# Performance work log

Hardware: AMD Instinct MI355X
Metric: run time of the kernel (lower is better)

Reference implementation:

```python
import jax, jax.numpy as jnp
import numpy as np

FACTOR = 0.1   # init_kwargs factor
EPS = 1e-7
B, C, H, W = 256, 3, 224, 224


def setup_inputs() -> dict:
    key = jax.random.key(0)
    k1, k2, k3 = jax.random.split(key, 3)
    x = jax.random.normal(k1, (B, C, H, W), dtype=jnp.float32)
    shift_fy = jax.random.uniform(k2, (B,), dtype=jnp.float32)  # maps to torch.rand(1)
    shift_fx = jax.random.uniform(k3, (B,), dtype=jnp.float32)
    return {"x": x, "shift_fy": shift_fy, "shift_fx": shift_fx}


def _shift_axis(img, shift, axis, size):
    # Equivalent to torch in-place slice copy + zero-fill:
    #   shift>0: img[..., :size-shift] = img[..., shift:]; img[..., size-shift:] = 0
    #   shift<0: img[..., -shift:]   = img[..., :shift];  img[..., :-shift]   = 0
    # == roll by -shift, then zero positions j where j+shift is out of [0, size)
    idx = jnp.arange(size)
    rolled = jnp.roll(img, -shift, axis=axis)
    mask = (idx + shift >= 0) & (idx + shift < size)
    shp = [1, 1, 1]
    shp[axis] = size
    return rolled * mask.reshape(shp).astype(img.dtype)


def _per_image(img, fy, fx):
    # img: [C, H, W]
    h, w = img.shape[1], img.shape[2]
    # int(shift_factor * size) truncates toward zero -> jnp.trunc
    sy = jnp.trunc((fy * 2.0 - 1.0) * FACTOR * h).astype(jnp.int32)
    sx = jnp.trunc((fx * 2.0 - 1.0) * FACTOR * w).astype(jnp.int32)
    img = _shift_axis(img, sy, 1, h)
    img = _shift_axis(img, sx, 2, w)
    # standardize with unbiased std (torch.std default, ddof=1)
    n = img.size
    mean = jnp.mean(img)
    var = jnp.sum(jnp.square(img - mean)) / (n - 1)
    img = (img - mean) / (jnp.sqrt(var) + EPS)
    # min-max normalize
    mn = jnp.min(img)
    mx = jnp.max(img)
    return (img - mn) / (mx - mn)


def reference(x, shift_fy, shift_fx):
    # fully vectorized over the batch (original uses a Python per-image loop)
    return jax.vmap(_per_image)(x, shift_fy, shift_fx)
```

## Files before the change

### kernel.cpp

```cpp
#include <hip/hip_runtime.h>
#include <math.h>


constexpr int kC = 3, kH = 224, kW = 224;
constexpr int kCHW  = kC * kH * kW;
constexpr int kROWS = kC * kH;
constexpr int kQPR  = kW / 4;
constexpr int TB    = 1024;
constexpr int WVB   = TB / 64;
constexpr int RPW   = kROWS / WVB;

typedef float f32x4 __attribute__((ext_vector_type(4)));

template <int NB>
__device__ __forceinline__ void p1_batch(const float* __restrict__ xb,
                                         int t0, int wv, int i0,
                                         const float* cm, int rlo, int rhi,
                                         float& vmin, float& vmax)
{
    f32x4 v[NB];
    #pragma unroll
    for (int u = 0; u < NB; ++u) {
        const int rr = wv + (t0 + u) * WVB;
        v[u] = *(const f32x4*)(xb + rr * kW + i0);
    }
    #pragma unroll
    for (int u = 0; u < NB; ++u) {
        const int rr = wv + (t0 + u) * WVB;
        const int j  = rr % kH;
        const float srm = (j >= rlo && j < rhi) ? 1.0f : 0.0f;
        #pragma unroll
        for (int k = 0; k < 4; ++k) {
            const float val = v[u][k] * cm[k] * srm;
            vmin = fminf(vmin, val);
            vmax = fmaxf(vmax, val);
        }
    }
}

template <int NB, int R>
__device__ __forceinline__ void p2_batch(const float* __restrict__ xb,
                                         float* __restrict__ ob,
                                         int t0, int wv, int i0, int qa, int qb,
                                         const float* cm, int sy,
                                         float inv, float zoff)
{
    f32x4 av[NB], bv[NB];
    #pragma unroll
    for (int u = 0; u < NB; ++u) {
        const int rr = wv + (t0 + u) * WVB;
        const int j  = rr % kH;
        const int jj = j + sy;
        const int jc = ((unsigned)jj < (unsigned)kH) ? jj : j;
        const float* __restrict__ src = xb + (rr - j + jc) * kW;
        av[u] = *(const f32x4*)(src + qa);
        bv[u] = *(const f32x4*)(src + qb);
    }
    #pragma unroll
    for (int u = 0; u < NB; ++u) {
        const int rr = wv + (t0 + u) * WVB;
        const int j  = rr % kH;
        const int jj = j + sy;
        const float scale = ((unsigned)jj < (unsigned)kH) ? inv : 0.0f;
        f32x4 o;
        #pragma unroll
        for (int k = 0; k < 4; ++k) {
            const float sel = (k + R < 4) ? av[u][k + R] : bv[u][k + R - 4];
            o[k] = fmaf(sel * cm[k], scale, zoff);
        }
        *(f32x4*)(ob + rr * kW + i0) = o;
    }
}

template <int R>
__device__ __forceinline__ void phase2(const float* __restrict__ xb,
                                       float* __restrict__ ob,
                                       int sy, int sx, float inv, float zoff,
                                       int wv, int lane)
{
    if (lane >= kQPR) return;
    const int i0   = lane * 4;
    const int base = i0 + sx - R;
    int qa = base;     qa = qa < 0 ? 0 : qa; qa = qa > kW - 4 ? kW - 4 : qa;
    int qb = base + 4; qb = qb < 0 ? 0 : qb; qb = qb > kW - 4 ? kW - 4 : qb;

    float cm[4];
    #pragma unroll
    for (int k = 0; k < 4; ++k)
        cm[k] = ((unsigned)(i0 + k + sx) < (unsigned)kW) ? 1.0f : 0.0f;

    for (int t0 = 0; t0 < RPW - 2; t0 += 4)
        p2_batch<4, R>(xb, ob, t0, wv, i0, qa, qb, cm, sy, inv, zoff);
    p2_batch<2, R>(xb, ob, RPW - 2, wv, i0, qa, qb, cm, sy, inv, zoff);
}

__global__ __launch_bounds__(TB) void shift_norm(
    const float* __restrict__ x, const float* __restrict__ sfy,
    const float* __restrict__ sfx, float* __restrict__ out)
{
    const int img = blockIdx.x;
    const float* __restrict__ xb = x + (size_t)img * kCHW;
    float* __restrict__ ob = out + (size_t)img * kCHW;

    float ty = sfy[img] * 2.0f - 1.0f; ty *= 0.1f; ty *= (float)kH;
    const int sy = (int)truncf(ty);
    float tx = sfx[img] * 2.0f - 1.0f; tx *= 0.1f; tx *= (float)kW;
    const int sx = (int)truncf(tx);

    const int rlo = sy > 0 ? sy : 0;
    const int rhi = kH + (sy < 0 ? sy : 0);
    const int clo = sx > 0 ? sx : 0;
    const int chi = kW + (sx < 0 ? sx : 0);

    const int tid  = threadIdx.x;
    const int lane = tid & 63;
    const int wv   = __builtin_amdgcn_readfirstlane(tid >> 6);

    const bool hasfill = (sy != 0) | (sx != 0);
    float vmin = hasfill ? 0.0f : INFINITY;
    float vmax = hasfill ? 0.0f : -INFINITY;

    if (lane < kQPR) {
        const int i0 = lane * 4;
        float cm[4];
        #pragma unroll
        for (int k = 0; k < 4; ++k)
            cm[k] = ((i0 + k) >= clo && (i0 + k) < chi) ? 1.0f : 0.0f;

        for (int t0 = 0; t0 < RPW - 2; t0 += 8)
            p1_batch<8>(xb, t0, wv, i0, cm, rlo, rhi, vmin, vmax);
        p1_batch<2>(xb, RPW - 2, wv, i0, cm, rlo, rhi, vmin, vmax);
    }

    #pragma unroll
    for (int off = 32; off > 0; off >>= 1) {
        vmin = fminf(vmin, __shfl_down(vmin, off));
        vmax = fmaxf(vmax, __shfl_down(vmax, off));
    }
    __shared__ float smin[WVB], smax[WVB];
    __shared__ float s_mn, s_inv;
    if (lane == 0) { smin[tid >> 6] = vmin; smax[tid >> 6] = vmax; }
    __syncthreads();
    if (tid == 0) {
        float mn = smin[0], mx = smax[0];
        #pragma unroll
        for (int w = 1; w < WVB; ++w) {
            mn = fminf(mn, smin[w]);
            mx = fmaxf(mx, smax[w]);
        }
        s_mn  = mn;
        s_inv = 1.0f / (mx - mn);
    }
    __syncthreads();
    const float mn   = s_mn;
    const float inv  = s_inv;
    const float zoff = (0.0f - mn) * inv;

    switch (sx & 3) {
        case 0: phase2<0>(xb, ob, sy, sx, inv, zoff, wv, lane); break;
        case 1: phase2<1>(xb, ob, sy, sx, inv, zoff, wv, lane); break;
        case 2: phase2<2>(xb, ob, sy, sx, inv, zoff, wv, lane); break;
        default: phase2<3>(xb, ob, sy, sx, inv, zoff, wv, lane); break;
    }
}

extern "C" void kernel_launch(void* const* d_in, const int* in_sizes, int n_in,
                              void* d_out, int out_size, void* d_ws, size_t ws_size,
                              hipStream_t stream) {
    const float* x  = (const float*)d_in[0];
    const float* fy = (const float*)d_in[1];
    const float* fx = (const float*)d_in[2];
    float* out = (float*)d_out;
    const int B = in_sizes[1];
    shift_norm<<<B, TB, 0, stream>>>(x, fy, fx, out);
}
```

Measured before the change: 299.5 us.

## Split each image across eight blocks with global atomic min/max rendezvous

Each image is now handled by eight 256-thread blocks instead of one 1024-thread block. Each block reduces min/max over its own row slice and publishes it through ordered-integer atomicMin/atomicMax in workspace. A spin-wait counter then makes all parts of an image see the global extremes before writing output. This raises the number of blocks to improve occupancy and balance, at the cost of two memsets per launch and a spin barrier. That barrier can deadlock if the parts of one image are not all co-resident.

```diff
diff --git a/kernel.cpp b/kernel.cpp
--- a/kernel.cpp
+++ b/kernel.cpp
@@ -6,77 +6,68 @@
 constexpr int kCHW  = kC * kH * kW;
 constexpr int kROWS = kC * kH;
 constexpr int kQPR  = kW / 4;
-constexpr int TB    = 1024;
+constexpr int TB    = 256;
+constexpr int PARTS = 8;
 constexpr int WVB   = TB / 64;
-constexpr int RPW   = kROWS / WVB;
+constexpr int RPW   = kROWS / (PARTS * WVB);
+constexpr int NB    = 7;
 
 typedef float f32x4 __attribute__((ext_vector_type(4)));
 
-template <int NB>
-__device__ __forceinline__ void p1_batch(const float* __restrict__ xb,
-                                         int t0, int wv, int i0,
-                                         const float* cm, int rlo, int rhi,
-                                         float& vmin, float& vmax)
-{
-    f32x4 v[NB];
+__device__ __forceinline__ unsigned enc_f(float f) {
+    const unsigned u = __float_as_uint(f);
+    return u ^ (((int)u >> 31) ? 0xFFFFFFFFu : 0x80000000u);
+}
+__device__ __forceinline__ float dec_f(unsigned e) {
+    return __uint_as_float(e ^ ((e & 0x80000000u) ? 0x80000000u : 0xFFFFFFFFu));
+}
+
+__device__ __forceinline__ void shifts_for(const float* __restrict__ sfy,
+                                           const float* __restrict__ sfx,
+                                           int img, int& sy, int& sx)
+{
+    float ty = sfy[img] * 2.0f - 1.0f; ty *= 0.1f; ty *= (float)kH;
+    sy = (int)truncf(ty);
+    float tx = sfx[img] * 2.0f - 1.0f; tx *= 0.1f; tx *= (float)kW;
+    sx = (int)truncf(tx);
+}
+
+__device__ __forceinline__ void phaseA_rows(const float* __restrict__ xb,
+                                            int r0, int rlo, int rhi,
+                                            int clo, int chi, int lane,
+                                            float& vmin, float& vmax)
+{
+    if (lane >= kQPR) return;
+    const int i0 = lane * 4;
+    float cm[4];
     #pragma unroll
-    for (int u = 0; u < NB; ++u) {
-        const int rr = wv + (t0 + u) * WVB;
-        v[u] = *(const f32x4*)(xb + rr * kW + i0);
-    }
-    #pragma unroll
-    for (int u = 0; u < NB; ++u) {
-        const int rr = wv + (t0 + u) * WVB;
-        const int j  = rr % kH;
-        const float srm = (j >= rlo && j < rhi) ? 1.0f : 0.0f;
-        #pragma unroll
-        for (int k = 0; k < 4; ++k) {
-            const float val = v[u][k] * cm[k] * srm;
-            vmin = fminf(vmin, val);
-            vmax = fmaxf(vmax, val);
-        }
-    }
-}
-
-template <int NB, int R>
-__device__ __forceinline__ void p2_batch(const float* __restrict__ xb,
-                                         float* __restrict__ ob,
-                                         int t0, int wv, int i0, int qa, int qb,
-                                         const float* cm, int sy,
-                                         float inv, float zoff)
-{
-    f32x4 av[NB], bv[NB];
-    #pragma unroll
-    for (int u = 0; u < NB; ++u) {
-        const int rr = wv + (t0 + u) * WVB;
-        const int j  = rr % kH;
-        const int jj = j + sy;
-        const int jc = ((unsigned)jj < (unsigned)kH) ? jj : j;
-        const float* __restrict__ src = xb + (rr - j + jc) * kW;
-        av[u] = *(const f32x4*)(src + qa);
-        bv[u] = *(const f32x4*)(src + qb);
-    }
-    #pragma unroll
-    for (int u = 0; u < NB; ++u) {
-        const int rr = wv + (t0 + u) * WVB;
-        const int j  = rr % kH;
-        const int jj = j + sy;
-        const float scale = ((unsigned)jj < (unsigned)kH) ? inv : 0.0f;
-        f32x4 o;
-        #pragma unroll
-        for (int k = 0; k < 4; ++k) {
-            const float sel = (k + R < 4) ? av[u][k + R] : bv[u][k + R - 4];
-            o[k] = fmaf(sel * cm[k], scale, zoff);
-        }
-        *(f32x4*)(ob + rr * kW + i0) = o;
+    for (int k = 0; k < 4; ++k)
+        cm[k] = ((i0 + k) >= clo && (i0 + k) < chi) ? 1.0f : 0.0f;
+
+    for (int t0 = 0; t0 < RPW; t0 += NB) {
+        f32x4 v[NB];
+        #pragma unroll
+        for (int u = 0; u < NB; ++u)
+            v[u] = *(const f32x4*)(xb + (r0 + t0 + u) * kW + i0);
+        #pragma unroll
+        for (int u = 0; u < NB; ++u) {
+            const int j = (r0 + t0 + u) % kH;
+            const float srm = (j >= rlo && j < rhi) ? 1.0f : 0.0f;
+            #pragma unroll
+            for (int k = 0; k < 4; ++k) {
+                const float val = v[u][k] * cm[k] * srm;
+                vmin = fminf(vmin, val);
+                vmax = fmaxf(vmax, val);
+            }
+        }
     }
 }
 
 template <int R>
-__device__ __forceinline__ void phase2(const float* __restrict__ xb,
-                                       float* __restrict__ ob,
-                                       int sy, int sx, float inv, float zoff,
-                                       int wv, int lane)
+__device__ __forceinline__ void phaseB_rows(const float* __restrict__ xb,
+                                            float* __restrict__ ob,
+                                            int r0, int sy, int sx,
+                                            float inv, float zoff, int lane)
 {
     if (lane >= kQPR) return;
     const int i0   = lane * 4;
@@ -89,23 +80,48 @@
     for (int k = 0; k < 4; ++k)
         cm[k] = ((unsigned)(i0 + k + sx) < (unsigned)kW) ? 1.0f : 0.0f;
 
-    for (int t0 = 0; t0 < RPW - 2; t0 += 4)
-        p2_batch<4, R>(xb, ob, t0, wv, i0, qa, qb, cm, sy, inv, zoff);
-    p2_batch<2, R>(xb, ob, RPW - 2, wv, i0, qa, qb, cm, sy, inv, zoff);
-}
-
-__global__ __launch_bounds__(TB) void shift_norm(
+    for (int t0 = 0; t0 < RPW; t0 += NB) {
+        f32x4 av[NB], bv[NB];
+        #pragma unroll
+        for (int u = 0; u < NB; ++u) {
+            const int rr = r0 + t0 + u;
+            const int j  = rr % kH;
+            const int jj = j + sy;
+            const int jc = ((unsigned)jj < (unsigned)kH) ? jj : j;
+            const float* __restrict__ src = xb + (rr - j + jc) * kW;
+            av[u] = *(const f32x4*)(src + qa);
+            bv[u] = *(const f32x4*)(src + qb);
+        }
+        #pragma unroll
+        for (int u = 0; u < NB; ++u) {
+            const int rr = r0 + t0 + u;
+            const int j  = rr % kH;
+            const int jj = j + sy;
+            const float scale = ((unsigned)jj < (unsigned)kH) ? inv : 0.0f;
+            f32x4 o;
+            #pragma unroll
+            for (int k = 0; k < 4; ++k) {
+                const float sel = (k + R < 4) ? av[u][k + R] : bv[u][k + R - 4];
+                o[k] = fmaf(sel * cm[k], scale, zoff);
+            }
+            *(f32x4*)(ob + rr * kW + i0) = o;
+        }
+    }
+}
+
+__global__ __launch_bounds__(TB) void shift_norm_pi(
     const float* __restrict__ x, const float* __restrict__ sfy,
-    const float* __restrict__ sfx, float* __restrict__ out)
-{
-    const int img = blockIdx.x;
+    const float* __restrict__ sfx, float* __restrict__ out,
+    unsigned* __restrict__ umin, unsigned* __restrict__ umax,
+    unsigned* __restrict__ cnt)
+{
+    const int gb   = blockIdx.x;
+    const int img  = gb >> 3;
+    const int part = gb & (PARTS - 1);
     const float* __restrict__ xb = x + (size_t)img * kCHW;
     float* __restrict__ ob = out + (size_t)img * kCHW;
 
-    float ty = sfy[img] * 2.0f - 1.0f; ty *= 0.1f; ty *= (float)kH;
-    const int sy = (int)truncf(ty);
-    float tx = sfx[img] * 2.0f - 1.0f; tx *= 0.1f; tx *= (float)kW;
-    const int sx = (int)truncf(tx);
+    int sy, sx; shifts_for(sfy, sfx, img, sy, sx);
 
     const int rlo = sy > 0 ? sy : 0;
     const int rhi = kH + (sy < 0 ? sy : 0);
@@ -115,22 +131,13 @@
     const int tid  = threadIdx.x;
     const int lane = tid & 63;
     const int wv   = __builtin_amdgcn_readfirstlane(tid >> 6);
+    const int r0   = part * (WVB * RPW) + wv * RPW;
 
     const bool hasfill = (sy != 0) | (sx != 0);
     float vmin = hasfill ? 0.0f : INFINITY;
     float vmax = hasfill ? 0.0f : -INFINITY;
 
-    if (lane < kQPR) {
-        const int i0 = lane * 4;
-        float cm[4];
-        #pragma unroll
-        for (int k = 0; k < 4; ++k)
-            cm[k] = ((i0 + k) >= clo && (i0 + k) < chi) ? 1.0f : 0.0f;
-
-        for (int t0 = 0; t0 < RPW - 2; t0 += 8)
-            p1_batch<8>(xb, t0, wv, i0, cm, rlo, rhi, vmin, vmax);
-        p1_batch<2>(xb, RPW - 2, wv, i0, cm, rlo, rhi, vmin, vmax);
-    }
+    phaseA_rows(xb, r0, rlo, rhi, clo, chi, lane, vmin, vmax);
 
     #pragma unroll
     for (int off = 32; off > 0; off >>= 1) {
@@ -148,8 +155,19 @@
             mn = fminf(mn, smin[w]);
             mx = fmaxf(mx, smax[w]);
         }
-        s_mn  = mn;
-        s_inv = 1.0f / (mx - mn);
+        atomicMin(&umin[img], enc_f(mn));
+        atomicMax(&umax[img], enc_f(mx));
+        __hip_atomic_fetch_add(&cnt[img], 1u, __ATOMIC_ACQ_REL,
+                               __HIP_MEMORY_SCOPE_AGENT);
+        while (__hip_atomic_load(&cnt[img], __ATOMIC_ACQUIRE,
+                                 __HIP_MEMORY_SCOPE_AGENT) < (unsigned)PARTS)
+            __builtin_amdgcn_s_sleep(4);
+        const float gmn = dec_f(__hip_atomic_load(&umin[img], __ATOMIC_RELAXED,
+                                                  __HIP_MEMORY_SCOPE_AGENT));
+        const float gmx = dec_f(__hip_atomic_load(&umax[img], __ATOMIC_RELAXED,
+                                                  __HIP_MEMORY_SCOPE_AGENT));
+        s_mn  = gmn;
+        s_inv = 1.0f / (gmx - gmn);
     }
     __syncthreads();
     const float mn   = s_mn;
@@ -157,10 +175,10 @@
     const float zoff = (0.0f - mn) * inv;
 
     switch (sx & 3) {
-        case 0: phase2<0>(xb, ob, sy, sx, inv, zoff, wv, lane); break;
-        case 1: phase2<1>(xb, ob, sy, sx, inv, zoff, wv, lane); break;
-        case 2: phase2<2>(xb, ob, sy, sx, inv, zoff, wv, lane); break;
-        default: phase2<3>(xb, ob, sy, sx, inv, zoff, wv, lane); break;
+        case 0: phaseB_rows<0>(xb, ob, r0, sy, sx, inv, zoff, lane); break;
+        case 1: phaseB_rows<1>(xb, ob, r0, sy, sx, inv, zoff, lane); break;
+        case 2: phaseB_rows<2>(xb, ob, r0, sy, sx, inv, zoff, lane); break;
+        default: phaseB_rows<3>(xb, ob, r0, sy, sx, inv, zoff, lane); break;
     }
 }
 
@@ -172,5 +190,12 @@
     const float* fx = (const float*)d_in[2];
     float* out = (float*)d_out;
     const int B = in_sizes[1];
-    shift_norm<<<B, TB, 0, stream>>>(x, fy, fx, out);
-}
+
+    unsigned* umin = (unsigned*)d_ws;
+    unsigned* umax = umin + B;
+    unsigned* cnt  = umax + B;
+    hipMemsetAsync(umin, 0xFF, (size_t)B * sizeof(unsigned), stream);
+    hipMemsetAsync(umax, 0x00, (size_t)B * 2 * sizeof(unsigned), stream);
+
+    shift_norm_pi<<<B * PARTS, TB, 0, stream>>>(x, fy, fx, out, umin, umax, cnt);
+}
```

Measured after the change: 426.9 us. 42.5% more time.
